# Kernel tuning notes

Measured on AMD Instinct MI355X. Metric: run time of the kernel, lower is better.

## Reference

```python
import jax, jax.numpy as jnp
import numpy as np

D_MODEL = 5120
N_HEADS = 8
D_HEAD = D_MODEL // N_HEADS          # 640
D_ROPE = 16
SPLIT_DIM = D_HEAD - D_ROPE          # 624
D_KV = 128
BATCH, SEQ = 2, 2048
ROPE_SCALE = 40.0


def _rope_cos_sin(seq_len):
    # inv_freq length = D_ROPE//4 (quirk of the original code)
    inv_freq = 1.0 / (10000.0 ** (jnp.arange(0, D_ROPE // 2, 2, dtype=jnp.float32) / (D_ROPE // 2)))
    t = jnp.arange(seq_len, dtype=jnp.float32) / ROPE_SCALE
    freqs = t[:, None] * inv_freq[None, :]            # [S, D_ROPE//4]
    emb = jnp.concatenate([freqs, freqs], axis=-1)    # [S, D_ROPE//2]
    cos = jnp.cos(emb)[None, :, None, :]              # [1,S,1,D_ROPE//2]
    sin = jnp.sin(emb)[None, :, None, :]
    return cos, sin


def _rotate_half(x):
    x1, x2 = jnp.split(x, 2, axis=-1)
    return jnp.concatenate([-x2, x1], axis=-1)


def _apply_rotary(x, cos, sin):
    r = cos.shape[-1]
    x_rot, x_base = x[..., :r], x[..., r:]
    x_rot = x_rot * cos + _rotate_half(x_rot) * sin
    return jnp.concatenate([x_rot, x_base], axis=-1)


def setup_inputs():
    key = jax.random.key(0)
    ks = jax.random.split(key, 18)
    s = 0.02
    inp = {
        'h': jax.random.normal(ks[0], (BATCH, SEQ, D_MODEL), dtype=jnp.float32),
        'W_dkv': jax.random.normal(ks[1], (D_MODEL, D_KV), dtype=jnp.float32) * s,
        'b_dkv': jnp.zeros((D_KV,), jnp.float32),
        'W_dq': jax.random.normal(ks[2], (D_MODEL, D_KV), dtype=jnp.float32) * s,
        'b_dq': jnp.zeros((D_KV,), jnp.float32),
        'W_uk': jax.random.normal(ks[3], (D_KV, N_HEADS * SPLIT_DIM), dtype=jnp.float32) * s,
        'b_uk': jnp.zeros((N_HEADS * SPLIT_DIM,), jnp.float32),
        'W_uv': jax.random.normal(ks[4], (D_KV, N_HEADS * D_HEAD), dtype=jnp.float32) * s,
        'b_uv': jnp.zeros((N_HEADS * D_HEAD,), jnp.float32),
        'W_uq': jax.random.normal(ks[5], (D_KV, N_HEADS * SPLIT_DIM), dtype=jnp.float32) * s,
        'b_uq': jnp.zeros((N_HEADS * SPLIT_DIM,), jnp.float32),
        'W_qr': jax.random.normal(ks[6], (D_KV, N_HEADS * D_ROPE), dtype=jnp.float32) * s,
        'b_qr': jnp.zeros((N_HEADS * D_ROPE,), jnp.float32),
        'W_kr': jax.random.normal(ks[7], (D_MODEL, N_HEADS * D_ROPE), dtype=jnp.float32) * s,
        'b_kr': jnp.zeros((N_HEADS * D_ROPE,), jnp.float32),
        'W_o': jax.random.normal(ks[8], (N_HEADS * D_HEAD, D_MODEL), dtype=jnp.float32) * s,
        'b_o': jnp.zeros((D_MODEL,), jnp.float32),
    }
    return inp


def reference(h, W_dkv, b_dkv, W_dq, b_dq, W_uk, b_uk, W_uv, b_uv,
              W_uq, b_uq, W_qr, b_qr, W_kr, b_kr, W_o, b_o):
    B, S, _ = h.shape
    c_kv = h @ W_dkv + b_dkv                                   # [B,S,D_KV]
    k = (c_kv @ W_uk + b_uk).reshape(B, S, N_HEADS, SPLIT_DIM)
    v = (c_kv @ W_uv + b_uv).reshape(B, S, N_HEADS, D_HEAD)
    c_q = h @ W_dq + b_dq
    q_base = (c_q @ W_uq + b_uq).reshape(B, S, N_HEADS, SPLIT_DIM)
    q_rot = (c_q @ W_qr + b_qr).reshape(B, S, N_HEADS, D_ROPE)
    cos, sin = _rope_cos_sin(S)
    q_rot = _apply_rotary(q_rot, cos, sin)
    k_rot = _apply_rotary((h @ W_kr + b_kr).reshape(B, S, N_HEADS, D_ROPE), cos, sin)
    q = jnp.concatenate([q_base, q_rot], axis=-1)              # [B,S,H,D_HEAD]
    k = jnp.concatenate([k, k_rot], axis=-1)                   # [B,S,H,D_HEAD]
    scores = jnp.einsum('bqhd,bkhd->bhqk', q, k) / jnp.sqrt(jnp.float32(D_HEAD))
    attn = jax.nn.softmax(scores, axis=-1)
    out = jnp.einsum('bhqk,bkhd->bqhd', attn, v)               # [B,S,H,D_HEAD]
    return out.reshape(B, S, N_HEADS * D_HEAD) @ W_o + b_o
```

## Files before the change

### kernel.cpp

```cpp
#include <hip/hip_runtime.h>


typedef unsigned short ushort_t;
typedef __attribute__((ext_vector_type(8)))  short          short8;
typedef __attribute__((ext_vector_type(8)))  unsigned short us8;
typedef __attribute__((ext_vector_type(4)))  float          f32x4;

#define SCALE_ATT 0.0395284707521047f

static __device__ inline unsigned short f2bf(float f) {
  union { float f; unsigned u; } v; v.f = f;
  unsigned r = (v.u + 0x7fffu + ((v.u >> 16) & 1u)) >> 16;
  return (unsigned short)r;
}
static __device__ inline float bf2f(unsigned short u) {
  union { unsigned u; float f; } v; v.u = ((unsigned)u) << 16;
  return v.f;
}
static __device__ inline f32x4 MFMA(short8 a, short8 b, f32x4 c) {
  return __builtin_amdgcn_mfma_f32_16x16x32_bf16(a, b, c, 0, 0, 0);
}

__global__ __launch_bounds__(256) void k_bvec_init(const float* __restrict__ bo,
                                                   float* __restrict__ bvec) {
  int n = blockIdx.x * 256 + threadIdx.x;
  bvec[n] = bo[n];
}

__global__ __launch_bounds__(128) void k_bqabs(const float* __restrict__ buq,
                                               const float* __restrict__ Wuk,
                                               float* __restrict__ bqabs) {
  int h = blockIdx.x, j = threadIdx.x;
  float acc = 0.f;
  const float* bq = buq + h * 624;
  const float* wk = Wuk + (size_t)j * 4992 + h * 624;
  for (int d = 0; d < 624; ++d) acc += bq[d] * wk[d];
  bqabs[h * 128 + j] = acc;
}

__global__ __launch_bounds__(256) void k_wqk(const float* __restrict__ Wuq,
                                             const float* __restrict__ Wuk,
                                             ushort_t* __restrict__ wqkT) {
  __shared__ float Aq[16 * 132];
  __shared__ float Ak[16 * 132];
  int jt = blockIdx.x, it = blockIdx.y, h = blockIdx.z;
  int i0 = it * 16, j0 = jt * 16;
  int t = threadIdx.x;
  int srow = t >> 4, sc0 = (t & 15) * 8;
  int ti = t & 15, tj = t >> 4;
  float acc = 0.f;
  for (int dc = 0; dc < 624; dc += 128) {
#pragma unroll
    for (int i = 0; i < 8; ++i) {
      int d = dc + sc0 + i;
      Aq[srow * 132 + sc0 + i] = (d < 624) ? Wuq[(size_t)(i0 + srow) * 4992 + h * 624 + d] : 0.f;
      Ak[srow * 132 + sc0 + i] = (d < 624) ? Wuk[(size_t)(j0 + srow) * 4992 + h * 624 + d] : 0.f;
    }
    __syncthreads();
    int cs = (624 - dc) < 128 ? (624 - dc) : 128;
    for (int d = 0; d < cs; d += 4) {
      const f32x4 a4 = *(const f32x4*)&Aq[ti * 132 + d];
      const f32x4 b4 = *(const f32x4*)&Ak[tj * 132 + d];
      acc += a4[0] * b4[0] + a4[1] * b4[1] + a4[2] * b4[2] + a4[3] * b4[3];
    }
    __syncthreads();
  }
  wqkT[(size_t)h * 16384 + (size_t)(j0 + tj) * 128 + (i0 + ti)] = f2bf(acc);
}

__global__ __launch_bounds__(256) void k_gemm1_sk(
    const float* __restrict__ H, const float* __restrict__ Wdkv,
    const float* __restrict__ Wdq, const float* __restrict__ Wkr,
    float* __restrict__ part) {
  __shared__ __align__(16) ushort_t As[64 * 72];
  __shared__ __align__(16) ushort_t Bs[192 * 72];
  const int tid = threadIdx.x;
  const int m0 = blockIdx.x * 64;
  const int n0 = blockIdx.y * 192;
  const int kc0 = blockIdx.z * 1280;
  const int lane = tid & 63, wid = tid >> 6;
  const int quad = lane >> 4, l15 = lane & 15;
  f32x4 acc[4][3];
#pragma unroll
  for (int a = 0; a < 4; ++a)
#pragma unroll
    for (int b = 0; b < 3; ++b) acc[a][b] = (f32x4){0.f, 0.f, 0.f, 0.f};
  const int ar = tid >> 2, ak0 = (tid & 3) * 16;
  const int br = tid >> 2, bsg = tid & 3;
  const int bkidx = br ^ (bsg << 4);
  const float* harow = H + (size_t)(m0 + ar) * 5120 + ak0;
  for (int kb = kc0; kb < kc0 + 1280; kb += 64) {
    const float* ap = harow + kb;
    us8 av0, av1;
#pragma unroll
    for (int i = 0; i < 8; ++i) { av0[i] = f2bf(ap[i]); av1[i] = f2bf(ap[8 + i]); }
    *(us8*)&As[ar * 72 + ak0] = av0;
    *(us8*)&As[ar * 72 + ak0 + 8] = av1;
#pragma unroll
    for (int g16 = 0; g16 < 3; ++g16) {
      const int lcol = g16 * 64 + bsg * 16;
      const int col = n0 + lcol;
      const float* base = (col < 128 ? Wdkv + col
                         : col < 256 ? Wdq + (col - 128)
                                     : Wkr + (col - 256)) + (size_t)(kb + br) * 128;
#pragma unroll
      for (int i = 0; i < 16; ++i)
        Bs[(lcol + i) * 72 + bkidx] = f2bf(base[i]);
    }
    __syncthreads();
#pragma unroll
    for (int ks = 0; ks < 2; ++ks) {
      short8 a[4], b[3];
#pragma unroll
      for (int mt = 0; mt < 4; ++mt)
        a[mt] = *(const short8*)&As[(mt * 16 + l15) * 72 + ks * 32 + quad * 8];
#pragma unroll
      for (int nt = 0; nt < 3; ++nt)
        b[nt] = *(const short8*)&Bs[(wid * 48 + nt * 16 + l15) * 72 +
                                    ((ks * 32 + quad * 8) ^ (((wid * 3 + nt) & 3) << 4))];
#pragma unroll
      for (int mt = 0; mt < 4; ++mt)
#pragma unroll
        for (int nt = 0; nt < 3; ++nt) acc[mt][nt] = MFMA(a[mt], b[nt], acc[mt][nt]);
    }
    __syncthreads();
  }
  const size_t pb = (size_t)blockIdx.z * 4096 * 384;
#pragma unroll
  for (int mt = 0; mt < 4; ++mt)
#pragma unroll
    for (int nt = 0; nt < 3; ++nt) {
      const int col = n0 + wid * 48 + nt * 16 + l15;
#pragma unroll
      for (int r = 0; r < 4; ++r) {
        const int row = m0 + mt * 16 + quad * 4 + r;
        part[pb + (size_t)row * 384 + col] = acc[mt][nt][r];
      }
    }
}

__global__ __launch_bounds__(384) void k_reduce(
    const float* __restrict__ part, const float* __restrict__ bdkv,
    const float* __restrict__ bdq, const float* __restrict__ bkr,
    ushort_t* __restrict__ ckv, ushort_t* __restrict__ cq,
    ushort_t* __restrict__ krot) {
  const int row = blockIdx.x;
  const int c = threadIdx.x;
  float v = 0.f;
#pragma unroll
  for (int ks = 0; ks < 4; ++ks)
    v += part[((size_t)ks * 4096 + row) * 384 + c];
  if (c < 128) {
    v += bdkv[c];
    ckv[(size_t)row * 128 + c] = f2bf(v);
  } else if (c < 256) {
    v += bdq[c - 128];
    cq[(size_t)row * 128 + (c - 128)] = f2bf(v);
  } else {
    v += bkr[c - 256];
    float partner = __shfl_xor(v, 4);
    const int j = (c - 256) & 15;
    const int head = (c - 256) >> 4;
    const int s = row & 2047, bb = row >> 11;
    const int j4 = j & 3;
    const float fr = (j4 == 0) ? 1.f : (j4 == 1) ? 0.1f : (j4 == 2) ? 0.01f : 0.001f;
    float sth, cth;
    __sincosf(s * 0.025f * fr, &sth, &cth);
    const float y = (j < 4) ? (v * cth - partner * sth)
                  : (j < 8) ? (v * cth + partner * sth) : v;
    krot[((size_t)((bb << 3) + head) * 2048 + s) * 16 + j] = f2bf(y);
  }
}

__global__ __launch_bounds__(256) void k_qrot(const ushort_t* __restrict__ cq,
                                              const float* __restrict__ Wqr,
                                              const float* __restrict__ bqr,
                                              ushort_t* __restrict__ qrot) {
  int gidx = blockIdx.x * 256 + threadIdx.x;
  int s = gidx & 2047, bh = gidx >> 11;
  int hh = bh & 7, bb = bh >> 3;
  const ushort_t* crow = cq + ((size_t)bb * 2048 + s) * 128;
  float acc[16];
#pragma unroll
  for (int j = 0; j < 16; ++j) acc[j] = bqr[hh * 16 + j];
  for (int k0 = 0; k0 < 128; k0 += 8) {
    us8 cv8 = *(const us8*)(crow + k0);
#pragma unroll
    for (int i = 0; i < 8; ++i) {
      float cv = bf2f(cv8[i]);
      const float* wr = Wqr + (size_t)(k0 + i) * 128 + hh * 16;
#pragma unroll
      for (int j = 0; j < 16; ++j) acc[j] += cv * wr[j];
    }
  }
  float y[16];
#pragma unroll
  for (int j4 = 0; j4 < 4; ++j4) {
    float fr = (j4 == 0) ? 1.f : (j4 == 1) ? 0.1f : (j4 == 2) ? 0.01f : 0.001f;
    float sth, cth;
    __sincosf(s * 0.025f * fr, &sth, &cth);
    y[j4] = acc[j4] * cth - acc[j4 + 4] * sth;
    y[j4 + 4] = acc[j4 + 4] * cth + acc[j4] * sth;
  }
#pragma unroll
  for (int j = 8; j < 16; ++j) y[j] = acc[j];
  us8 o0, o1;
#pragma unroll
  for (int j = 0; j < 8; ++j) {
    o0[j] = f2bf(y[j] * SCALE_ATT);
    o1[j] = f2bf(y[8 + j] * SCALE_ATT);
  }
  *(us8*)(qrot + (size_t)gidx * 16) = o0;
  *(us8*)(qrot + (size_t)gidx * 16 + 8) = o1;
}

__global__ __launch_bounds__(256) void k_qabs(const ushort_t* __restrict__ cq,
                                              const ushort_t* __restrict__ wqkT,
                                              const float* __restrict__ bqabs,
                                              ushort_t* __restrict__ qabs) {
  __shared__ __align__(16) ushort_t As[128 * 72];
  __shared__ __align__(16) ushort_t Bs[128 * 72];
  const int tid = threadIdx.x;
  const int m0 = blockIdx.x * 128, hh = blockIdx.y;
  const int lane = tid & 63, wid = tid >> 6;
  const int quad = lane >> 4, l15 = lane & 15;
  const int wm = wid & 1, wn = wid >> 1;
  f32x4 acc[4][4];
#pragma unroll
  for (int a = 0; a < 4; ++a)
#pragma unroll
    for (int b = 0; b < 4; ++b) acc[a][b] = (f32x4){0.f, 0.f, 0.f, 0.f};
  const int ar = tid >> 1, as0 = (tid & 1) * 32;
  for (int kb = 0; kb < 128; kb += 64) {
    const ushort_t* ap = cq + (size_t)(m0 + ar) * 128 + kb + as0;
    const ushort_t* bp = wqkT + (size_t)hh * 16384 + (size_t)ar * 128 + kb + as0;
#pragma unroll
    for (int w = 0; w < 4; ++w) {
      *(us8*)&As[ar * 72 + as0 + w * 8] = *(const us8*)(ap + w * 8);
      *(us8*)&Bs[ar * 72 + as0 + w * 8] = *(const us8*)(bp + w * 8);
    }
    __syncthreads();
#pragma unroll
    for (int ks = 0; ks < 2; ++ks) {
      short8 a[4], b[4];
#pragma unroll
      for (int mt = 0; mt < 4; ++mt)
        a[mt] = *(const short8*)&As[(wm * 64 + mt * 16 + l15) * 72 + ks * 32 + quad * 8];
#pragma unroll
      for (int nt = 0; nt < 4; ++nt)
        b[nt] = *(const short8*)&Bs[(wn * 64 + nt * 16 + l15) * 72 + ks * 32 + quad * 8];
#pragma unroll
      for (int mt = 0; mt < 4; ++mt)
#pragma unroll
        for (int nt = 0; nt < 4; ++nt) acc[mt][nt] = MFMA(a[mt], b[nt], acc[mt][nt]);
    }
    __syncthreads();
  }
#pragma unroll
  for (int mt = 0; mt < 4; ++mt)
#pragma unroll
    for (int nt = 0; nt < 4; ++nt) {
      int col = wn * 64 + nt * 16 + l15;
      float bias = bqabs[hh * 128 + col];
#pragma unroll
      for (int r = 0; r < 4; ++r) {
        int m = m0 + wm * 64 + mt * 16 + quad * 4 + r;
        int bb = m >> 11, s = m & 2047;
        qabs[((size_t)((bb << 3) + hh) * 2048 + s) * 128 + col] =
            f2bf((acc[mt][nt][r] + bias) * SCALE_ATT);
      }
    }
}

__global__ __launch_bounds__(256) void k_comb(const float* __restrict__ Wo,
                                              const float* __restrict__ Wuv,
                                              const float* __restrict__ buv,
                                              ushort_t* __restrict__ wcombT,
                                              float* __restrict__ bvec) {
  __shared__ __align__(16) ushort_t As[128 * 72];
  __shared__ __align__(16) ushort_t Bs[128 * 72];
  const int tid = threadIdx.x;
  const int n0 = blockIdx.x * 128, hh = blockIdx.y;
  const int lane = tid & 63, wid = tid >> 6;
  const int quad = lane >> 4, l15 = lane & 15;
  const int wm = wid & 1, wn = wid >> 1;
  f32x4 acc[4][4];
#pragma unroll
  for (int a = 0; a < 4; ++a)
#pragma unroll
    for (int b = 0; b < 4; ++b) acc[a][b] = (f32x4){0.f, 0.f, 0.f, 0.f};
  const int ad = tid >> 2, asg = tid & 3;
  const int an0 = asg * 32;
  const int akidx = ad ^ (asg << 4);
  const int bc = tid >> 1, bd0 = (tid & 1) * 32;
  const int bvc = tid >> 1, bvh = tid & 1;
  const int bsgr = (bvc >> 5) & 3;
  const float* buvh = buv + hh * 640;
  float bacc = 0.f;
  for (int kb = 0; kb < 640; kb += 64) {
    const float* ap = Wo + (size_t)(hh * 640 + kb + ad) * 5120 + n0 + an0;
#pragma unroll
    for (int i = 0; i < 32; ++i) As[(an0 + i) * 72 + akidx] = f2bf(ap[i]);
    const float* bp = Wuv + (size_t)bc * 5120 + hh * 640 + kb + bd0;
    us8 bv0, bv1, bv2, bv3;
#pragma unroll
    for (int i = 0; i < 8; ++i) {
      bv0[i] = f2bf(bp[i]); bv1[i] = f2bf(bp[8 + i]);
      bv2[i] = f2bf(bp[16 + i]); bv3[i] = f2bf(bp[24 + i]);
    }
    *(us8*)&Bs[bc * 72 + bd0] = bv0;
    *(us8*)&Bs[bc * 72 + bd0 + 8] = bv1;
    *(us8*)&Bs[bc * 72 + bd0 + 16] = bv2;
    *(us8*)&Bs[bc * 72 + bd0 + 24] = bv3;
    __syncthreads();
#pragma unroll
    for (int d8 = 0; d8 < 4; ++d8) {
      const int k0 = bvh * 32 + d8 * 8;
      const us8 a8 = *(const us8*)&As[bvc * 72 + (k0 ^ (bsgr << 4))];
      const f32x4 b4a = *(const f32x4*)&buvh[kb + k0];
      const f32x4 b4b = *(const f32x4*)&buvh[kb + k0 + 4];
      bacc += b4a[0] * bf2f(a8[0]) + b4a[1] * bf2f(a8[1]) +
              b4a[2] * bf2f(a8[2]) + b4a[3] * bf2f(a8[3]) +
              b4b[0] * bf2f(a8[4]) + b4b[1] * bf2f(a8[5]) +
              b4b[2] * bf2f(a8[6]) + b4b[3] * bf2f(a8[7]);
    }
#pragma unroll
    for (int ks = 0; ks < 2; ++ks) {
      short8 a[4], b[4];
#pragma unroll
      for (int mt = 0; mt < 4; ++mt)
        a[mt] = *(const short8*)&As[(wm * 64 + mt * 16 + l15) * 72 +
                                    ((ks * 32 + quad * 8) ^ (((wm * 2 + (mt >> 1)) & 3) << 4))];
#pragma unroll
      for (int nt = 0; nt < 4; ++nt)
        b[nt] = *(const short8*)&Bs[(wn * 64 + nt * 16 + l15) * 72 + ks * 32 + quad * 8];
#pragma unroll
      for (int mt = 0; mt < 4; ++mt)
#pragma unroll
        for (int nt = 0; nt < 4; ++nt) acc[mt][nt] = MFMA(a[mt], b[nt], acc[mt][nt]);
    }
    __syncthreads();
  }
#pragma unroll
  for (int mt = 0; mt < 4; ++mt)
#pragma unroll
    for (int nt = 0; nt < 4; ++nt) {
      int col = wn * 64 + nt * 16 + l15;
#pragma unroll
      for (int r = 0; r < 4; ++r) {
        int n = n0 + wm * 64 + mt * 16 + quad * 4 + r;
        wcombT[(size_t)n * 1024 + hh * 128 + col] = f2bf(acc[mt][nt][r]);
      }
    }
  atomicAdd(&bvec[n0 + bvc], bacc);
}

__global__ __launch_bounds__(256) void k_attn(const ushort_t* __restrict__ qabs,
                                              const ushort_t* __restrict__ qrot,
                                              const ushort_t* __restrict__ ckv,
                                              const ushort_t* __restrict__ krot,
                                              ushort_t* __restrict__ ctx) {
  __shared__ __align__(16) ushort_t Qs[64 * 168];
  __shared__ __align__(16) ushort_t Ks[64 * 168];
  __shared__ __align__(16) ushort_t Vt[128 * 72];
  __shared__ __align__(16) ushort_t Ps[64 * 72];
  const int tid = threadIdx.x;
  const int bh = blockIdx.y, bb = bh >> 3, hh = bh & 7;
  const int q0 = blockIdx.x * 64;
  const int lane = tid & 63, wid = tid >> 6;
  const int quad = lane >> 4, l15 = lane & 15;
  const int sr = tid >> 2, sseg = tid & 3;
  (void)hh;
  {
    const ushort_t* qa = qabs + ((size_t)bh * 2048 + q0 + sr) * 128 + sseg * 32;
#pragma unroll
    for (int w = 0; w < 4; ++w)
      *(us8*)&Qs[sr * 168 + sseg * 32 + w * 8] = *(const us8*)(qa + w * 8);
    if (sseg == 0) {
      const ushort_t* qr = qrot + ((size_t)bh * 2048 + q0 + sr) * 16;
      *(us8*)&Qs[sr * 168 + 128] = *(const us8*)qr;
      *(us8*)&Qs[sr * 168 + 136] = *(const us8*)(qr + 8);
    }
    if (sseg == 1) {
      us8 z = (us8)0;
      *(us8*)&Qs[sr * 168 + 144] = z;
      *(us8*)&Qs[sr * 168 + 152] = z;
    }
  }
  f32x4 oacc[8];
#pragma unroll
  for (int i = 0; i < 8; ++i) oacc[i] = (f32x4){0.f, 0.f, 0.f, 0.f};
  float mrow[4] = {-1e30f, -1e30f, -1e30f, -1e30f};
  float lrow[4] = {0.f, 0.f, 0.f, 0.f};

  for (int kt = 0; kt < 32; ++kt) {
    int key0 = kt * 64;
    {
      const ushort_t* kp = ckv + ((size_t)bb * 2048 + key0 + sr) * 128 + sseg * 32;
      us8 v[4];
#pragma unroll
      for (int w = 0; w < 4; ++w) v[w] = *(const us8*)(kp + w * 8);
#pragma unroll
      for (int w = 0; w < 4; ++w)
        *(us8*)&Ks[sr * 168 + sseg * 32 + w * 8] = v[w];
      const int vc = sr ^ (sseg << 4);
#pragma unroll
      for (int w = 0; w < 4; ++w)
#pragma unroll
        for (int i = 0; i < 8; ++i)
          Vt[(sseg * 32 + w * 8 + i) * 72 + vc] = v[w][i];
      if (sseg == 0) {
        const ushort_t* kr = krot + ((size_t)bh * 2048 + key0 + sr) * 16;
        *(us8*)&Ks[sr * 168 + 128] = *(const us8*)kr;
        *(us8*)&Ks[sr * 168 + 136] = *(const us8*)(kr + 8);
      }
      if (sseg == 1) {
        us8 z = (us8)0;
        *(us8*)&Ks[sr * 168 + 144] = z;
        *(us8*)&Ks[sr * 168 + 152] = z;
      }
    }
    __syncthreads();
    f32x4 sacc[4];
#pragma unroll
    for (int nt = 0; nt < 4; ++nt) sacc[nt] = (f32x4){0.f, 0.f, 0.f, 0.f};
#pragma unroll
    for (int ks = 0; ks < 5; ++ks) {
      short8 aq = *(const short8*)&Qs[(wid * 16 + l15) * 168 + ks * 32 + quad * 8];
#pragma unroll
      for (int nt = 0; nt < 4; ++nt) {
        short8 bk = *(const short8*)&Ks[(nt * 16 + l15) * 168 + ks * 32 + quad * 8];
        sacc[nt] = MFMA(aq, bk, sacc[nt]);
      }
    }
    float p[4][4];
#pragma unroll
    for (int r = 0; r < 4; ++r) {
      float mx = fmaxf(fmaxf(sacc[0][r], sacc[1][r]), fmaxf(sacc[2][r], sacc[3][r]));
#pragma unroll
      for (int off = 1; off < 16; off <<= 1) mx = fmaxf(mx, __shfl_xor(mx, off));
      if (mx > mrow[r]) {
        float alpha = __expf(mrow[r] - mx);
        mrow[r] = mx;
        lrow[r] *= alpha;
#pragma unroll
        for (int t8 = 0; t8 < 8; ++t8) oacc[t8][r] *= alpha;
      }
      float rs = 0.f;
#pragma unroll
      for (int nt = 0; nt < 4; ++nt) {
        float pv = __expf(sacc[nt][r] - mrow[r]);
        p[nt][r] = pv;
        rs += pv;
      }
      lrow[r] += rs;
    }
#pragma unroll
    for (int nt = 0; nt < 4; ++nt)
#pragma unroll
      for (int r = 0; r < 4; ++r)
        Ps[(wid * 16 + quad * 4 + r) * 72 + nt * 16 + l15] = f2bf(p[nt][r]);
    __syncthreads();
#pragma unroll
    for (int kk = 0; kk < 2; ++kk) {
      short8 pa = *(const short8*)&Ps[(wid * 16 + l15) * 72 + kk * 32 + quad * 8];
#pragma unroll
      for (int nt = 0; nt < 8; ++nt) {
        short8 vb = *(const short8*)&Vt[(nt * 16 + l15) * 72 +
                                        ((kk * 32 + quad * 8) ^ ((nt >> 1) << 4))];
        oacc[nt] = MFMA(pa, vb, oacc[nt]);
      }
    }
    __syncthreads();
  }
#pragma unroll
  for (int r = 0; r < 4; ++r) {
#pragma unroll
    for (int off = 1; off < 16; off <<= 1) lrow[r] += __shfl_xor(lrow[r], off);
    float rl = 1.f / lrow[r];
    int row = q0 + wid * 16 + quad * 4 + r;
    size_t base = ((size_t)bb * 2048 + row) * 1024 + hh * 128;
#pragma unroll
    for (int nt = 0; nt < 8; ++nt)
      ctx[base + nt * 16 + l15] = f2bf(oacc[nt][r] * rl);
  }
}

__global__ __launch_bounds__(256) void k_final(const ushort_t* __restrict__ ctx,
                                               const ushort_t* __restrict__ wcombT,
                                               const float* __restrict__ bvec,
                                               float* __restrict__ out) {
  __shared__ __align__(16) ushort_t As[128 * 72];
  __shared__ __align__(16) ushort_t Bs[128 * 72];
  const int tid = threadIdx.x;
  const int m0 = blockIdx.x * 128, n0 = blockIdx.y * 128;
  const int lane = tid & 63, wid = tid >> 6;
  const int quad = lane >> 4, l15 = lane & 15;
  const int wm = wid & 1, wn = wid >> 1;
  f32x4 acc[4][4];
#pragma unroll
  for (int a = 0; a < 4; ++a)
#pragma unroll
    for (int b = 0; b < 4; ++b) acc[a][b] = (f32x4){0.f, 0.f, 0.f, 0.f};
  const int ar = tid >> 1, as0 = (tid & 1) * 32;
  for (int kb = 0; kb < 1024; kb += 64) {
    const ushort_t* ap = ctx + (size_t)(m0 + ar) * 1024 + kb + as0;
    const ushort_t* bp = wcombT + (size_t)(n0 + ar) * 1024 + kb + as0;
#pragma unroll
    for (int w = 0; w < 4; ++w) {
      *(us8*)&As[ar * 72 + as0 + w * 8] = *(const us8*)(ap + w * 8);
      *(us8*)&Bs[ar * 72 + as0 + w * 8] = *(const us8*)(bp + w * 8);
    }
    __syncthreads();
#pragma unroll
    for (int ks = 0; ks < 2; ++ks) {
      short8 a[4], b[4];
#pragma unroll
      for (int mt = 0; mt < 4; ++mt)
        a[mt] = *(const short8*)&As[(wm * 64 + mt * 16 + l15) * 72 + ks * 32 + quad * 8];
#pragma unroll
      for (int nt = 0; nt < 4; ++nt)
        b[nt] = *(const short8*)&Bs[(wn * 64 + nt * 16 + l15) * 72 + ks * 32 + quad * 8];
#pragma unroll
      for (int mt = 0; mt < 4; ++mt)
#pragma unroll
        for (int nt = 0; nt < 4; ++nt) acc[mt][nt] = MFMA(a[mt], b[nt], acc[mt][nt]);
    }
    __syncthreads();
  }
#pragma unroll
  for (int mt = 0; mt < 4; ++mt)
#pragma unroll
    for (int nt = 0; nt < 4; ++nt) {
      int col = wn * 64 + nt * 16 + l15;
      float bias = bvec[n0 + col];
#pragma unroll
      for (int r = 0; r < 4; ++r) {
        int row = m0 + wm * 64 + mt * 16 + quad * 4 + r;
        out[(size_t)row * 5120 + n0 + col] = acc[mt][nt][r] + bias;
      }
    }
}

extern "C" void kernel_launch(void* const* d_in, const int* in_sizes, int n_in,
                              void* d_out, int out_size, void* d_ws, size_t ws_size,
                              hipStream_t stream) {
  const float* H    = (const float*)d_in[0];
  const float* Wdkv = (const float*)d_in[1];
  const float* bdkv = (const float*)d_in[2];
  const float* Wdq  = (const float*)d_in[3];
  const float* bdq  = (const float*)d_in[4];
  const float* Wuk  = (const float*)d_in[5];
  const float* Wuv  = (const float*)d_in[7];
  const float* buv  = (const float*)d_in[8];
  const float* Wuq  = (const float*)d_in[9];
  const float* buq  = (const float*)d_in[10];
  const float* Wqr  = (const float*)d_in[11];
  const float* bqr  = (const float*)d_in[12];
  const float* Wkr  = (const float*)d_in[13];
  const float* bkr  = (const float*)d_in[14];
  const float* Wo   = (const float*)d_in[15];
  const float* bo   = (const float*)d_in[16];
  float* out = (float*)d_out;

  char* ws = (char*)d_ws;
  size_t off = 0;
  auto alloc = [&](size_t bytes) -> void* {
    void* p = ws + off;
    off += (bytes + 255) & ~(size_t)255;
    return p;
  };
  ushort_t* ckv    = (ushort_t*)alloc((size_t)4096 * 128 * 2);
  ushort_t* cq     = (ushort_t*)alloc((size_t)4096 * 128 * 2);
  ushort_t* krot   = (ushort_t*)alloc((size_t)16 * 2048 * 16 * 2);
  ushort_t* qrot   = (ushort_t*)alloc((size_t)16 * 2048 * 16 * 2);
  ushort_t* wqkT   = (ushort_t*)alloc((size_t)8 * 128 * 128 * 2);
  float*    bqabs  = (float*)alloc((size_t)8 * 128 * 4);
  float*    bvec   = (float*)alloc((size_t)5120 * 4);
  size_t mark = off;
  float*    part   = (float*)alloc((size_t)4 * 4096 * 384 * 4);
  size_t endB = off;
  off = mark;
  ushort_t* qabs   = (ushort_t*)alloc((size_t)16 * 2048 * 128 * 2);
  ushort_t* wcombT = (ushort_t*)alloc((size_t)5120 * 1024 * 2);
  ushort_t* ctx    = (ushort_t*)alloc((size_t)4096 * 1024 * 2);
  if (off < endB) off = endB;
  (void)ws_size; (void)in_sizes; (void)n_in; (void)out_size;

  hipLaunchKernelGGL(k_bvec_init, dim3(20), dim3(256), 0, stream, bo, bvec);
  hipLaunchKernelGGL(k_bqabs, dim3(8), dim3(128), 0, stream, buq, Wuk, bqabs);
  hipLaunchKernelGGL(k_wqk, dim3(8, 8, 8), dim3(256), 0, stream, Wuq, Wuk, wqkT);
  hipLaunchKernelGGL(k_gemm1_sk, dim3(64, 2, 4), dim3(256), 0, stream,
                     H, Wdkv, Wdq, Wkr, part);
  hipLaunchKernelGGL(k_reduce, dim3(4096), dim3(384), 0, stream,
                     part, bdkv, bdq, bkr, ckv, cq, krot);
  hipLaunchKernelGGL(k_comb, dim3(40, 8), dim3(256), 0, stream, Wo, Wuv, buv, wcombT, bvec);
  hipLaunchKernelGGL(k_qrot, dim3(128), dim3(256), 0, stream, cq, Wqr, bqr, qrot);
  hipLaunchKernelGGL(k_qabs, dim3(32, 8), dim3(256), 0, stream, cq, wqkT, bqabs, qabs);
  hipLaunchKernelGGL(k_attn, dim3(32, 16), dim3(256), 0, stream, qabs, qrot, ckv, krot, ctx);
  hipLaunchKernelGGL(k_final, dim3(32, 40), dim3(256), 0, stream, ctx, wcombT, bvec, out);
}
```

Baseline: 693.1 us.

## Pretranspose latent KV, register-prefetch next tiles in attention and final GEMM

Adds a small kernel that writes a transposed copy of the latent KV (ckvT), so the attention kernel fills its V tile with vector stores instead of scalar transposed LDS writes. The attention and final GEMM loops now prefetch the next K/V (or A/B) tile into registers while MFMAs on the current tile run. P is converted with packed bf16 conversion, and the constant zero padding of Ks is written once instead of every iteration. This costs an extra launch, another workspace buffer and more register pressure, which may reduce occupancy.

```diff
diff --git a/kernel.cpp b/kernel.cpp
--- a/kernel.cpp
+++ b/kernel.cpp
@@ -16,6 +16,11 @@
 static __device__ inline float bf2f(unsigned short u) {
   union { unsigned u; float f; } v; v.u = ((unsigned)u) << 16;
   return v.f;
+}
+static __device__ inline unsigned cvt_pk_bf16(float a, float b) {
+  unsigned r;
+  asm("v_cvt_pk_bf16_f32 %0, %1, %2" : "=v"(r) : "v"(a), "v"(b));
+  return r;
 }
 static __device__ inline f32x4 MFMA(short8 a, short8 b, f32x4 c) {
   return __builtin_amdgcn_mfma_f32_16x16x32_bf16(a, b, c, 0, 0, 0);
@@ -172,6 +177,33 @@
   }
 }
 
+__global__ __launch_bounds__(256) void k_ckvt(const ushort_t* __restrict__ ckv,
+                                              ushort_t* __restrict__ ckvT) {
+  __shared__ __align__(16) ushort_t T[128 * 72];
+  const int tid = threadIdx.x;
+  const int s0 = blockIdx.x * 64;
+  const int bb = s0 >> 11, sl = s0 & 2047;
+  const int sr = tid >> 2, sseg = tid & 3;
+  {
+    const ushort_t* kp = ckv + ((size_t)s0 + sr) * 128 + sseg * 32;
+    us8 v[4];
+#pragma unroll
+    for (int w = 0; w < 4; ++w) v[w] = *(const us8*)(kp + w * 8);
+#pragma unroll
+    for (int w = 0; w < 4; ++w)
+#pragma unroll
+      for (int i = 0; i < 8; ++i)
+        T[(sseg * 32 + w * 8 + i) * 72 + sr] = v[w][i];
+  }
+  __syncthreads();
+  const int vrow = tid >> 1, vk0 = (tid & 1) * 32;
+#pragma unroll
+  for (int w = 0; w < 4; ++w) {
+    us8 t = *(const us8*)&T[vrow * 72 + vk0 + w * 8];
+    *(us8*)(ckvT + ((size_t)bb * 128 + vrow) * 2048 + sl + vk0 + w * 8) = t;
+  }
+}
+
 __global__ __launch_bounds__(256) void k_qrot(const ushort_t* __restrict__ cq,
                                               const float* __restrict__ Wqr,
                                               const float* __restrict__ bqr,
@@ -359,6 +391,7 @@
                                               const ushort_t* __restrict__ qrot,
                                               const ushort_t* __restrict__ ckv,
                                               const ushort_t* __restrict__ krot,
+                                              const ushort_t* __restrict__ ckvT,
                                               ushort_t* __restrict__ ctx) {
   __shared__ __align__(16) ushort_t Qs[64 * 168];
   __shared__ __align__(16) ushort_t Ks[64 * 168];
@@ -370,6 +403,7 @@
   const int lane = tid & 63, wid = tid >> 6;
   const int quad = lane >> 4, l15 = lane & 15;
   const int sr = tid >> 2, sseg = tid & 3;
+  const int vrow = tid >> 1, vk0 = (tid & 1) * 32;
   (void)hh;
   {
     const ushort_t* qa = qabs + ((size_t)bh * 2048 + q0 + sr) * 128 + sseg * 32;
@@ -385,8 +419,25 @@
       us8 z = (us8)0;
       *(us8*)&Qs[sr * 168 + 144] = z;
       *(us8*)&Qs[sr * 168 + 152] = z;
-    }
-  }
+      *(us8*)&Ks[sr * 168 + 144] = z;
+      *(us8*)&Ks[sr * 168 + 152] = z;
+    }
+  }
+  us8 kreg[4], vreg[4], krr0, krr1;
+  auto loadKV = [&](int key0) {
+    const ushort_t* kp = ckv + ((size_t)bb * 2048 + key0 + sr) * 128 + sseg * 32;
+#pragma unroll
+    for (int w = 0; w < 4; ++w) kreg[w] = *(const us8*)(kp + w * 8);
+    const ushort_t* vp = ckvT + ((size_t)bb * 128 + vrow) * 2048 + key0 + vk0;
+#pragma unroll
+    for (int w = 0; w < 4; ++w) vreg[w] = *(const us8*)(vp + w * 8);
+    if (sseg == 0) {
+      const ushort_t* kr = krot + ((size_t)bh * 2048 + key0 + sr) * 16;
+      krr0 = *(const us8*)kr;
+      krr1 = *(const us8*)(kr + 8);
+    }
+  };
+  loadKV(0);
   f32x4 oacc[8];
 #pragma unroll
   for (int i = 0; i < 8; ++i) oacc[i] = (f32x4){0.f, 0.f, 0.f, 0.f};
@@ -394,32 +445,16 @@
   float lrow[4] = {0.f, 0.f, 0.f, 0.f};
 
   for (int kt = 0; kt < 32; ++kt) {
-    int key0 = kt * 64;
-    {
-      const ushort_t* kp = ckv + ((size_t)bb * 2048 + key0 + sr) * 128 + sseg * 32;
-      us8 v[4];
-#pragma unroll
-      for (int w = 0; w < 4; ++w) v[w] = *(const us8*)(kp + w * 8);
-#pragma unroll
-      for (int w = 0; w < 4; ++w)
-        *(us8*)&Ks[sr * 168 + sseg * 32 + w * 8] = v[w];
-      const int vc = sr ^ (sseg << 4);
-#pragma unroll
-      for (int w = 0; w < 4; ++w)
-#pragma unroll
-        for (int i = 0; i < 8; ++i)
-          Vt[(sseg * 32 + w * 8 + i) * 72 + vc] = v[w][i];
-      if (sseg == 0) {
-        const ushort_t* kr = krot + ((size_t)bh * 2048 + key0 + sr) * 16;
-        *(us8*)&Ks[sr * 168 + 128] = *(const us8*)kr;
-        *(us8*)&Ks[sr * 168 + 136] = *(const us8*)(kr + 8);
-      }
-      if (sseg == 1) {
-        us8 z = (us8)0;
-        *(us8*)&Ks[sr * 168 + 144] = z;
-        *(us8*)&Ks[sr * 168 + 152] = z;
-      }
-    }
+#pragma unroll
+    for (int w = 0; w < 4; ++w)
+      *(us8*)&Ks[sr * 168 + sseg * 32 + w * 8] = kreg[w];
+    if (sseg == 0) {
+      *(us8*)&Ks[sr * 168 + 128] = krr0;
+      *(us8*)&Ks[sr * 168 + 136] = krr1;
+    }
+#pragma unroll
+    for (int w = 0; w < 4; ++w)
+      *(us8*)&Vt[vrow * 72 + vk0 + w * 8] = vreg[w];
     __syncthreads();
     f32x4 sacc[4];
 #pragma unroll
@@ -433,6 +468,7 @@
         sacc[nt] = MFMA(aq, bk, sacc[nt]);
       }
     }
+    if (kt < 31) loadKV((kt + 1) * 64);
     float p[4][4];
 #pragma unroll
     for (int r = 0; r < 4; ++r) {
@@ -458,16 +494,19 @@
 #pragma unroll
     for (int nt = 0; nt < 4; ++nt)
 #pragma unroll
-      for (int r = 0; r < 4; ++r)
-        Ps[(wid * 16 + quad * 4 + r) * 72 + nt * 16 + l15] = f2bf(p[nt][r]);
+      for (int rp = 0; rp < 2; ++rp) {
+        unsigned pk = cvt_pk_bf16(p[nt][2 * rp], p[nt][2 * rp + 1]);
+        int ad = (wid * 16 + quad * 4 + 2 * rp) * 72 + nt * 16 + l15;
+        Ps[ad] = (ushort_t)pk;
+        Ps[ad + 72] = (ushort_t)(pk >> 16);
+      }
     __syncthreads();
 #pragma unroll
     for (int kk = 0; kk < 2; ++kk) {
       short8 pa = *(const short8*)&Ps[(wid * 16 + l15) * 72 + kk * 32 + quad * 8];
 #pragma unroll
       for (int nt = 0; nt < 8; ++nt) {
-        short8 vb = *(const short8*)&Vt[(nt * 16 + l15) * 72 +
-                                        ((kk * 32 + quad * 8) ^ ((nt >> 1) << 4))];
+        short8 vb = *(const short8*)&Vt[(nt * 16 + l15) * 72 + kk * 32 + quad * 8];
         oacc[nt] = MFMA(pa, vb, oacc[nt]);
       }
     }
@@ -503,15 +542,30 @@
 #pragma unroll
     for (int b = 0; b < 4; ++b) acc[a][b] = (f32x4){0.f, 0.f, 0.f, 0.f};
   const int ar = tid >> 1, as0 = (tid & 1) * 32;
+  const ushort_t* ap = ctx + (size_t)(m0 + ar) * 1024 + as0;
+  const ushort_t* bp = wcombT + (size_t)(n0 + ar) * 1024 + as0;
+  us8 ra[4], rb[4];
+#pragma unroll
+  for (int w = 0; w < 4; ++w) {
+    ra[w] = *(const us8*)(ap + w * 8);
+    rb[w] = *(const us8*)(bp + w * 8);
+  }
   for (int kb = 0; kb < 1024; kb += 64) {
-    const ushort_t* ap = ctx + (size_t)(m0 + ar) * 1024 + kb + as0;
-    const ushort_t* bp = wcombT + (size_t)(n0 + ar) * 1024 + kb + as0;
 #pragma unroll
     for (int w = 0; w < 4; ++w) {
-      *(us8*)&As[ar * 72 + as0 + w * 8] = *(const us8*)(ap + w * 8);
-      *(us8*)&Bs[ar * 72 + as0 + w * 8] = *(const us8*)(bp + w * 8);
-    }
-    __syncthreads();
+      *(us8*)&As[ar * 72 + as0 + w * 8] = ra[w];
+      *(us8*)&Bs[ar * 72 + as0 + w * 8] = rb[w];
+    }
+    __syncthreads();
+    if (kb < 960) {
+      const ushort_t* ap2 = ap + kb + 64;
+      const ushort_t* bp2 = bp + kb + 64;
+#pragma unroll
+      for (int w = 0; w < 4; ++w) {
+        ra[w] = *(const us8*)(ap2 + w * 8);
+        rb[w] = *(const us8*)(bp2 + w * 8);
+      }
+    }
 #pragma unroll
     for (int ks = 0; ks < 2; ++ks) {
       short8 a[4], b[4];
@@ -572,6 +626,7 @@
   };
   ushort_t* ckv    = (ushort_t*)alloc((size_t)4096 * 128 * 2);
   ushort_t* cq     = (ushort_t*)alloc((size_t)4096 * 128 * 2);
+  ushort_t* ckvT   = (ushort_t*)alloc((size_t)2 * 128 * 2048 * 2);
   ushort_t* krot   = (ushort_t*)alloc((size_t)16 * 2048 * 16 * 2);
   ushort_t* qrot   = (ushort_t*)alloc((size_t)16 * 2048 * 16 * 2);
   ushort_t* wqkT   = (ushort_t*)alloc((size_t)8 * 128 * 128 * 2);
@@ -594,9 +649,11 @@
                      H, Wdkv, Wdq, Wkr, part);
   hipLaunchKernelGGL(k_reduce, dim3(4096), dim3(384), 0, stream,
                      part, bdkv, bdq, bkr, ckv, cq, krot);
+  hipLaunchKernelGGL(k_ckvt, dim3(64), dim3(256), 0, stream, ckv, ckvT);
   hipLaunchKernelGGL(k_comb, dim3(40, 8), dim3(256), 0, stream, Wo, Wuv, buv, wcombT, bvec);
   hipLaunchKernelGGL(k_qrot, dim3(128), dim3(256), 0, stream, cq, Wqr, bqr, qrot);
   hipLaunchKernelGGL(k_qabs, dim3(32, 8), dim3(256), 0, stream, cq, wqkT, bqabs, qabs);
-  hipLaunchKernelGGL(k_attn, dim3(32, 16), dim3(256), 0, stream, qabs, qrot, ckv, krot, ctx);
+  hipLaunchKernelGGL(k_attn, dim3(32, 16), dim3(256), 0, stream,
+                     qabs, qrot, ckv, krot, ckvT, ctx);
   hipLaunchKernelGGL(k_final, dim3(32, 40), dim3(256), 0, stream, ctx, wcombT, bvec, out);
 }
```

Measured after the change: 679.7 us. About the same (-1.9%).
